# Kernel optimization log

Hardware: AMD Instinct MI355X
Metric: run time of the kernel (lower is better)

Reference implementation:

```python
import jax, jax.numpy as jnp
import numpy as np

COMMIT_W = 0.25
EMA_DECAY = 0.99
EPS = 1e-5


def setup_inputs() -> dict:
    key = jax.random.key(0)
    k1, k2 = jax.random.split(key)
    B, T, D, K = 16, 1024, 512, 8192
    features = jax.random.normal(k1, (B, T, D), dtype=jnp.float32)
    # __init__ does uniform_(-1/K, 1/K) then ema_weight.copy_(embeddings)
    embeddings = jax.random.uniform(k2, (K, D), dtype=jnp.float32, minval=-1.0 / K, maxval=1.0 / K)
    ema_weight = embeddings
    ema_cluster_size = jnp.ones((K,), dtype=jnp.float32)
    return {"features": features, "embeddings": embeddings,
            "ema_cluster_size": ema_cluster_size, "ema_weight": ema_weight}


def reference(features, embeddings, ema_cluster_size, ema_weight):
    B, T, D = features.shape
    K = embeddings.shape[0]
    flat = features.reshape(-1, D)                      # [N, D]
    # Squared-distance expansion; argmin is identical to argmin of cdist.
    d2 = (jnp.sum(flat * flat, axis=1, keepdims=True)
          - 2.0 * flat @ embeddings.T
          + jnp.sum(embeddings * embeddings, axis=1))   # [N, K]
    indices = jnp.argmin(d2, axis=1)                    # [N]
    quantized = embeddings[indices].reshape(B, T, D)
    # Straight-through estimator
    quantized_st = features + jax.lax.stop_gradient(quantized - features)
    commitment = jnp.mean((features - jax.lax.stop_gradient(quantized_st)) ** 2)
    extra_losses = COMMIT_W * commitment
    # EMA codebook update (training mode); scatter-add instead of one-hot matmul
    ones = jnp.ones(indices.shape, dtype=flat.dtype)
    cluster_size = jax.ops.segment_sum(ones, indices, num_segments=K)          # [K]
    embed_sum = jax.ops.segment_sum(jax.lax.stop_gradient(flat), indices,
                                    num_segments=K)                            # [K, D]
    new_cs = EMA_DECAY * ema_cluster_size + (1.0 - EMA_DECAY) * cluster_size
    new_w = EMA_DECAY * ema_weight + (1.0 - EMA_DECAY) * embed_sum
    cs_norm = (new_cs + EPS) / (jnp.sum(new_cs) + K * EPS)
    new_embeddings = new_w / cs_norm[:, None]
    targets = indices.reshape(B, T)
    return quantized_st, targets, extra_losses, new_embeddings, new_cs, new_w
```

## Files before the change

kernel.cpp:

```cpp
#include <hip/hip_runtime.h>

typedef unsigned short u16;
typedef unsigned int   u32;
typedef unsigned long long u64;

constexpr int NROW  = 16384;
constexpr int DIM   = 512;
constexpr int KCODE = 8192;

constexpr int BM   = 128;
constexpr int BN   = 128;
constexpr int BK   = 32;
constexpr int LSTR = 36;

constexpr size_t Q_OFF = 0;
constexpr size_t T_OFF = 8388608;
constexpr size_t L_OFF = 8404992;
constexpr size_t E_OFF = 8404993;
constexpr size_t C_OFF = 12599297;
constexpr size_t W_OFF = 12607489;

constexpr size_t WS_KEYS   = 0;
constexpr size_t WS_CSIZE  = 131072;
constexpr size_t WS_COMMIT = 163840;
constexpr size_t WS_CSSUM  = 163844;
constexpr size_t WS_XNORM  = 196608;
constexpr size_t WS_ENORM  = 262144;
constexpr size_t WS_ESUM   = 327680;
constexpr size_t WS_NEEDED = WS_ESUM + (size_t)KCODE * DIM * 4;

__global__ void rownorm_kernel(const float* __restrict__ src, float* __restrict__ dst) {
    #pragma clang fp contract(off)
    __shared__ float s[4][DIM];
    __shared__ float rr[4][32];
    const int wave = threadIdx.x >> 6, lane = threadIdx.x & 63;
    const int row = blockIdx.x * 4 + wave;
    const float4* p = (const float4*)(src + (size_t)row * DIM);
    float4 v0 = p[lane];
    float4 v1 = p[lane + 64];
    *(float4*)&s[wave][lane * 4] = v0;
    *(float4*)&s[wave][(lane + 64) * 4] = v1;
    __syncthreads();
    if (lane < 32) {
        const int b = lane >> 3, j = lane & 7;
        const float* q = &s[wave][b * 128 + j];
        float x = q[0];
        float r = x * x;
        for (int t = 1; t < 16; ++t) {
            float y = q[8 * t];
            float py = y * y;
            r = r + py;
        }
        rr[wave][lane] = r;
    }
    __syncthreads();
    if (lane == 0) {
        const float* R = rr[wave];
        float B0 = ((R[0] + R[1]) + (R[2] + R[3])) + ((R[4] + R[5]) + (R[6] + R[7]));
        float B1 = ((R[8] + R[9]) + (R[10] + R[11])) + ((R[12] + R[13]) + (R[14] + R[15]));
        float B2 = ((R[16] + R[17]) + (R[18] + R[19])) + ((R[20] + R[21]) + (R[22] + R[23]));
        float B3 = ((R[24] + R[25]) + (R[26] + R[27])) + ((R[28] + R[29]) + (R[30] + R[31]));
        dst[row] = (B0 + B1) + (B2 + B3);
    }
}

typedef short bf16x8 __attribute__((ext_vector_type(8)));
typedef float f32x16 __attribute__((ext_vector_type(16)));

__device__ __forceinline__ bf16x8 ld_frag(const u16* p) {
    uint2 a = *(const uint2*)p;
    uint2 b = *(const uint2*)(p + 4);
    int4 t = make_int4((int)a.x, (int)a.y, (int)b.x, (int)b.y);
    return __builtin_bit_cast(bf16x8, t);
}

__device__ __forceinline__ u32 bf16rne(float x) {
    u32 u = __float_as_uint(x);
    return (u + 0x7fffu + ((u >> 16) & 1u)) >> 16;
}

__device__ __forceinline__ void split4(float4 v, u32& hp0, u32& hp1, u32& lp0, u32& lp1) {
    u32 h0 = bf16rne(v.x), h1 = bf16rne(v.y), h2 = bf16rne(v.z), h3 = bf16rne(v.w);
    hp0 = h0 | (h1 << 16);
    hp1 = h2 | (h3 << 16);
    float r0 = v.x - __uint_as_float(h0 << 16);
    float r1 = v.y - __uint_as_float(h1 << 16);
    float r2 = v.z - __uint_as_float(h2 << 16);
    float r3 = v.w - __uint_as_float(h3 << 16);
    lp0 = bf16rne(r0) | (bf16rne(r1) << 16);
    lp1 = bf16rne(r2) | (bf16rne(r3) << 16);
}

__device__ __forceinline__ u64 packkey(float v, int code) {
    u32 vb = __float_as_uint(v);
    vb = (vb & 0x80000000u) ? ~vb : (vb | 0x80000000u);
    return ((u64)vb << 32) | (u32)code;
}

__launch_bounds__(256, 3)
__global__ void argmin_kernel(const float* __restrict__ feat,
                              const float* __restrict__ emb,
                              const float* __restrict__ xnorm,
                              const float* __restrict__ enorm,
                              u64* __restrict__ keys) {
    __shared__ u16 sAh[BM][LSTR], sAl[BM][LSTR], sBh[BN][LSTR], sBl[BN][LSTR];
    __shared__ float sXn[BM], sEn[BN];

    const int tid = threadIdx.x;
    const int swz = ((int)blockIdx.x & 7) * 1024 + ((int)blockIdx.x >> 3);
    const int cp = swz & 63;
    const int rp = swz >> 6;
    const int row0 = rp * BM;
    const int code0 = cp * BN;

    if (tid < BM) sXn[tid] = xnorm[row0 + tid];
    else          sEn[tid - BM] = enorm[code0 + (tid - BM)];

    const int srow = tid >> 3;
    const int scol = (tid & 7) * 4;
    const float* aBase = feat + (size_t)row0 * DIM;
    const float* bBase = emb + (size_t)code0 * DIM;

    float4 pa[4], pb[4];
    #pragma unroll
    for (int l = 0; l < 4; ++l) {
        pa[l] = *(const float4*)&aBase[(size_t)(srow + 32 * l) * DIM + scol];
        pb[l] = *(const float4*)&bBase[(size_t)(srow + 32 * l) * DIM + scol];
    }

    const int lane = tid & 63;
    const int wv = tid >> 6;
    const int wr = wv & 1, wc = wv >> 1;
    const int c5 = lane & 31, hgrp = lane >> 5;

    f32x16 acc[2][2] = {};

    #pragma unroll 1
    for (int kt = 0; kt < DIM / BK; ++kt) {
        __syncthreads();
        #pragma unroll
        for (int l = 0; l < 4; ++l) {
            u32 h0, h1, q0, q1;
            split4(pa[l], h0, h1, q0, q1);
            *(uint2*)&sAh[srow + 32 * l][scol] = make_uint2(h0, h1);
            *(uint2*)&sAl[srow + 32 * l][scol] = make_uint2(q0, q1);
            split4(pb[l], h0, h1, q0, q1);
            *(uint2*)&sBh[srow + 32 * l][scol] = make_uint2(h0, h1);
            *(uint2*)&sBl[srow + 32 * l][scol] = make_uint2(q0, q1);
        }
        __syncthreads();
        if (kt + 1 < DIM / BK) {
            const int k0 = (kt + 1) * BK;
            #pragma unroll
            for (int l = 0; l < 4; ++l) {
                pa[l] = *(const float4*)&aBase[(size_t)(srow + 32 * l) * DIM + k0 + scol];
                pb[l] = *(const float4*)&bBase[(size_t)(srow + 32 * l) * DIM + k0 + scol];
            }
        }
        #pragma unroll
        for (int s = 0; s < 2; ++s) {
            const int kk = s * 16 + hgrp * 8;
            bf16x8 ah[2], al[2], bh[2], bl[2];
            #pragma unroll
            for (int i = 0; i < 2; ++i) {
                ah[i] = ld_frag(&sAh[64 * wr + 32 * i + c5][kk]);
                al[i] = ld_frag(&sAl[64 * wr + 32 * i + c5][kk]);
                bh[i] = ld_frag(&sBh[64 * wc + 32 * i + c5][kk]);
                bl[i] = ld_frag(&sBl[64 * wc + 32 * i + c5][kk]);
            }
            #pragma unroll
            for (int i = 0; i < 2; ++i) {
                #pragma unroll
                for (int j = 0; j < 2; ++j) {
                    acc[i][j] = __builtin_amdgcn_mfma_f32_32x32x16_bf16(ah[i], bh[j], acc[i][j], 0, 0, 0);
                    acc[i][j] = __builtin_amdgcn_mfma_f32_32x32x16_bf16(ah[i], bl[j], acc[i][j], 0, 0, 0);
                    acc[i][j] = __builtin_amdgcn_mfma_f32_32x32x16_bf16(al[i], bh[j], acc[i][j], 0, 0, 0);
                }
            }
        }
    }

    #pragma unroll
    for (int i = 0; i < 2; ++i) {
        #pragma unroll
        for (int r = 0; r < 16; ++r) {
            const int rowt = 64 * wr + 32 * i + (r & 3) + 8 * (r >> 2) + 4 * hgrp;
            const float xv = sXn[rowt];
            const int ct0 = 64 * wc + c5;
            float v0 = fmaf(-2.0f, acc[i][0][r], xv) + sEn[ct0];
            float v1 = fmaf(-2.0f, acc[i][1][r], xv) + sEn[ct0 + 32];
            u64 ka = packkey(v0, code0 + ct0);
            u64 kb = packkey(v1, code0 + ct0 + 32);
            u64 key = (kb < ka) ? kb : ka;
            #pragma unroll
            for (int m = 1; m < 32; m <<= 1) {
                u64 o = __shfl_xor(key, m, 64);
                if (o < key) key = o;
            }
            if (c5 == 0) atomicMin(&keys[row0 + rowt], key);
        }
    }
}

__global__ void gather_kernel(const float* __restrict__ feat,
                              const float* __restrict__ emb,
                              const unsigned long long* __restrict__ keys,
                              float* __restrict__ qout,
                              float* __restrict__ targets,
                              float* __restrict__ esum,
                              float* __restrict__ csize,
                              float* __restrict__ commit) {
    const int row = blockIdx.x;
    const int code = (int)(keys[row] & 0x7fffffffu);
    const int d = threadIdx.x * 2;
    float2 f = *(const float2*)&feat[(size_t)row * DIM + d];
    float2 q = *(const float2*)&emb[(size_t)code * DIM + d];
    float2 qst;
    qst.x = f.x + (q.x - f.x);
    qst.y = f.y + (q.y - f.y);
    *(float2*)&qout[(size_t)row * DIM + d] = qst;
    float dx = f.x - qst.x, dy = f.y - qst.y;
    float local = dx * dx + dy * dy;
    #pragma unroll
    for (int off = 32; off; off >>= 1) local += __shfl_down(local, off, 64);
    __shared__ float wsum[4];
    int lane = threadIdx.x & 63, wv = threadIdx.x >> 6;
    if (lane == 0) wsum[wv] = local;
    __syncthreads();
    if (threadIdx.x == 0) {
        atomicAdd(commit, wsum[0] + wsum[1] + wsum[2] + wsum[3]);
        atomicAdd(&csize[code], 1.0f);
        targets[row] = (float)code;
    }
    atomicAdd(&esum[(size_t)code * DIM + d], f.x);
    atomicAdd(&esum[(size_t)code * DIM + d + 1], f.y);
}

__global__ void newcs_kernel(const float* __restrict__ ema_cs,
                             const float* __restrict__ csize,
                             float* __restrict__ out_cs,
                             float* __restrict__ cs_sum,
                             const float* __restrict__ commit,
                             float* __restrict__ out_loss) {
    int i = blockIdx.x * 256 + threadIdx.x;
    float v = 0.99f * ema_cs[i] + 0.01f * csize[i];
    out_cs[i] = v;
    float s = v;
    #pragma unroll
    for (int off = 32; off; off >>= 1) s += __shfl_down(s, off, 64);
    __shared__ float wsum[4];
    int lane = threadIdx.x & 63, wv = threadIdx.x >> 6;
    if (lane == 0) wsum[wv] = s;
    __syncthreads();
    if (threadIdx.x == 0)
        atomicAdd(cs_sum, wsum[0] + wsum[1] + wsum[2] + wsum[3]);
    if (blockIdx.x == 0 && threadIdx.x == 0)
        out_loss[0] = 0.25f * commit[0] / 8388608.0f;
}

__global__ void final_kernel(const float* __restrict__ ema_w,
                             const float* __restrict__ esum,
                             const float* __restrict__ new_cs,
                             const float* __restrict__ cs_sum,
                             float* __restrict__ out_w,
                             float* __restrict__ out_emb) {
    size_t i4 = ((size_t)blockIdx.x * 256 + threadIdx.x) * 4;
    int k = (int)(i4 >> 9);
    float S = cs_sum[0] + (float)KCODE * 1e-5f;
    float4 es = *(const float4*)&esum[i4];
    float4 ew = *(const float4*)&ema_w[i4];
    float w0 = 0.99f * ew.x + 0.01f * es.x;
    float w1 = 0.99f * ew.y + 0.01f * es.y;
    float w2 = 0.99f * ew.z + 0.01f * es.z;
    float w3 = 0.99f * ew.w + 0.01f * es.w;
    out_w[i4 + 0] = w0; out_w[i4 + 1] = w1; out_w[i4 + 2] = w2; out_w[i4 + 3] = w3;
    float scale = S / (new_cs[k] + 1e-5f);
    out_emb[i4 + 0] = w0 * scale; out_emb[i4 + 1] = w1 * scale;
    out_emb[i4 + 2] = w2 * scale; out_emb[i4 + 3] = w3 * scale;
}

extern "C" void kernel_launch(void* const* d_in, const int* in_sizes, int n_in,
                              void* d_out, int out_size, void* d_ws, size_t ws_size,
                              hipStream_t stream) {
    const float* feat   = (const float*)d_in[0];
    const float* emb    = (const float*)d_in[1];
    const float* ema_cs = (const float*)d_in[2];
    const float* ema_w  = (const float*)d_in[3];
    float* out = (float*)d_out;
    char* ws = (char*)d_ws;
    if (ws_size < WS_NEEDED) return;

    u64* keys     = (u64*)(ws + WS_KEYS);
    float* csize  = (float*)(ws + WS_CSIZE);
    float* commit = (float*)(ws + WS_COMMIT);
    float* cssum  = (float*)(ws + WS_CSSUM);
    float* xnorm  = (float*)(ws + WS_XNORM);
    float* enorm  = (float*)(ws + WS_ENORM);
    float* esum   = (float*)(ws + WS_ESUM);

    (void)hipMemsetAsync(ws + WS_KEYS, 0xFF, (size_t)NROW * 8, stream);
    (void)hipMemsetAsync(ws + WS_CSIZE, 0, WS_CSSUM + 4 - WS_CSIZE, stream);
    (void)hipMemsetAsync(ws + WS_ESUM, 0, (size_t)KCODE * DIM * 4, stream);

    rownorm_kernel<<<NROW / 4, 256, 0, stream>>>(feat, xnorm);
    rownorm_kernel<<<KCODE / 4, 256, 0, stream>>>(emb, enorm);
    argmin_kernel<<<(NROW / BM) * (KCODE / BN), 256, 0, stream>>>(feat, emb, xnorm, enorm, keys);
    gather_kernel<<<NROW, 256, 0, stream>>>(feat, emb, keys, out + Q_OFF, out + T_OFF,
                                            esum, csize, commit);
    newcs_kernel<<<KCODE / 256, 256, 0, stream>>>(ema_cs, csize, out + C_OFF, cssum, commit, out + L_OFF);
    final_kernel<<<KCODE * DIM / 1024, 256, 0, stream>>>(ema_w, esum, out + C_OFF, cssum,
                                                         out + W_OFF, out + E_OFF);
}
```

Baseline: 1.028 ms.

## Pre-split inputs into bf16 hi/lo buffers before the argmin GEMM

```diff
diff --git a/kernel.cpp b/kernel.cpp
--- a/kernel.cpp
+++ b/kernel.cpp
@@ -28,6 +28,11 @@
 constexpr size_t WS_ENORM  = 262144;
 constexpr size_t WS_ESUM   = 327680;
 constexpr size_t WS_NEEDED = WS_ESUM + (size_t)KCODE * DIM * 4;
+constexpr size_t WS_FH = WS_NEEDED;
+constexpr size_t WS_FL = WS_FH + (size_t)NROW * DIM * 2;
+constexpr size_t WS_EH = WS_FL + (size_t)NROW * DIM * 2;
+constexpr size_t WS_EL = WS_EH + (size_t)KCODE * DIM * 2;
+constexpr size_t WS_BIG = WS_EL + (size_t)KCODE * DIM * 2;
 
 __global__ void rownorm_kernel(const float* __restrict__ src, float* __restrict__ dst) {
     #pragma clang fp contract(off)
@@ -67,10 +72,7 @@
 typedef short bf16x8 __attribute__((ext_vector_type(8)));
 typedef float f32x16 __attribute__((ext_vector_type(16)));
 
-__device__ __forceinline__ bf16x8 ld_frag(const u16* p) {
-    uint2 a = *(const uint2*)p;
-    uint2 b = *(const uint2*)(p + 4);
-    int4 t = make_int4((int)a.x, (int)a.y, (int)b.x, (int)b.y);
+__device__ __forceinline__ bf16x8 frag_of(int4 t) {
     return __builtin_bit_cast(bf16x8, t);
 }
 
@@ -97,12 +99,135 @@
     return ((u64)vb << 32) | (u32)code;
 }
 
+__global__ void split_kernel(const float* __restrict__ src,
+                             u16* __restrict__ hi, u16* __restrict__ lo) {
+    const size_t i = (size_t)blockIdx.x * 256 + threadIdx.x;
+    const float4* p = (const float4*)src;
+    float4 a = p[i * 2], b = p[i * 2 + 1];
+    u32 ah0, ah1, al0, al1, bh0, bh1, bl0, bl1;
+    split4(a, ah0, ah1, al0, al1);
+    split4(b, bh0, bh1, bl0, bl1);
+    ((uint4*)hi)[i] = make_uint4(ah0, ah1, bh0, bh1);
+    ((uint4*)lo)[i] = make_uint4(al0, al1, bl0, bl1);
+}
+
 __launch_bounds__(256, 3)
-__global__ void argmin_kernel(const float* __restrict__ feat,
-                              const float* __restrict__ emb,
-                              const float* __restrict__ xnorm,
-                              const float* __restrict__ enorm,
-                              u64* __restrict__ keys) {
+__global__ void argmin_ps_kernel(const u16* __restrict__ fH, const u16* __restrict__ fL,
+                                 const u16* __restrict__ eH, const u16* __restrict__ eL,
+                                 const float* __restrict__ xnorm,
+                                 const float* __restrict__ enorm,
+                                 u64* __restrict__ keys) {
+    __shared__ int4 sAh[512], sAl[512], sBh[512], sBl[512];
+    __shared__ float sXn[BM], sEn[BN];
+
+    const int tid = threadIdx.x;
+    const int swz = ((int)blockIdx.x & 7) * 1024 + ((int)blockIdx.x >> 3);
+    const int cp = swz & 63;
+    const int rp = swz >> 6;
+    const int row0 = rp * BM;
+    const int code0 = cp * BN;
+
+    if (tid < BM) sXn[tid] = xnorm[row0 + tid];
+    else          sEn[tid - BM] = enorm[code0 + (tid - BM)];
+
+    const int k8l = tid & 3;
+    const int c5s = (tid >> 2) & 31;
+    const int rbs = tid >> 7;
+    const int4* fH4 = (const int4*)fH;
+    const int4* fL4 = (const int4*)fL;
+    const int4* eH4 = (const int4*)eH;
+    const int4* eL4 = (const int4*)eL;
+    const size_t rowA = (size_t)(row0 + rbs * 32 + c5s);
+    const size_t rowB = (size_t)(code0 + rbs * 32 + c5s);
+    const int ldsIdx0 = rbs * 128 + k8l * 32 + c5s;
+
+    int4 pAh[2], pAl[2], pBh[2], pBl[2];
+    #pragma unroll
+    for (int r = 0; r < 2; ++r) {
+        const size_t ia = (rowA + 64 * r) * 64 + k8l;
+        const size_t ib = (rowB + 64 * r) * 64 + k8l;
+        pAh[r] = fH4[ia]; pAl[r] = fL4[ia];
+        pBh[r] = eH4[ib]; pBl[r] = eL4[ib];
+    }
+
+    const int lane = tid & 63;
+    const int wv = tid >> 6;
+    const int wr = wv & 1, wc = wv >> 1;
+    const int c5 = lane & 31, hgrp = lane >> 5;
+
+    f32x16 acc[2][2] = {};
+
+    #pragma unroll 1
+    for (int kt = 0; kt < DIM / BK; ++kt) {
+        __syncthreads();
+        #pragma unroll
+        for (int r = 0; r < 2; ++r) {
+            sAh[ldsIdx0 + 256 * r] = pAh[r];
+            sAl[ldsIdx0 + 256 * r] = pAl[r];
+            sBh[ldsIdx0 + 256 * r] = pBh[r];
+            sBl[ldsIdx0 + 256 * r] = pBl[r];
+        }
+        __syncthreads();
+        if (kt + 1 < DIM / BK) {
+            #pragma unroll
+            for (int r = 0; r < 2; ++r) {
+                const size_t ia = (rowA + 64 * r) * 64 + (kt + 1) * 4 + k8l;
+                const size_t ib = (rowB + 64 * r) * 64 + (kt + 1) * 4 + k8l;
+                pAh[r] = fH4[ia]; pAl[r] = fL4[ia];
+                pBh[r] = eH4[ib]; pBl[r] = eL4[ib];
+            }
+        }
+        #pragma unroll
+        for (int s = 0; s < 2; ++s) {
+            const int k8 = s * 2 + hgrp;
+            bf16x8 ah[2], al[2], bh[2], bl[2];
+            #pragma unroll
+            for (int i = 0; i < 2; ++i) {
+                ah[i] = frag_of(sAh[((2 * wr + i) * 4 + k8) * 32 + c5]);
+                al[i] = frag_of(sAl[((2 * wr + i) * 4 + k8) * 32 + c5]);
+                bh[i] = frag_of(sBh[((2 * wc + i) * 4 + k8) * 32 + c5]);
+                bl[i] = frag_of(sBl[((2 * wc + i) * 4 + k8) * 32 + c5]);
+            }
+            #pragma unroll
+            for (int i = 0; i < 2; ++i) {
+                #pragma unroll
+                for (int j = 0; j < 2; ++j) {
+                    acc[i][j] = __builtin_amdgcn_mfma_f32_32x32x16_bf16(ah[i], bh[j], acc[i][j], 0, 0, 0);
+                    acc[i][j] = __builtin_amdgcn_mfma_f32_32x32x16_bf16(ah[i], bl[j], acc[i][j], 0, 0, 0);
+                    acc[i][j] = __builtin_amdgcn_mfma_f32_32x32x16_bf16(al[i], bh[j], acc[i][j], 0, 0, 0);
+                }
+            }
+        }
+    }
+
+    #pragma unroll
+    for (int i = 0; i < 2; ++i) {
+        #pragma unroll
+        for (int r = 0; r < 16; ++r) {
+            const int rowt = 64 * wr + 32 * i + (r & 3) + 8 * (r >> 2) + 4 * hgrp;
+            const float xv = sXn[rowt];
+            const int ct0 = 64 * wc + c5;
+            float v0 = fmaf(-2.0f, acc[i][0][r], xv) + sEn[ct0];
+            float v1 = fmaf(-2.0f, acc[i][1][r], xv) + sEn[ct0 + 32];
+            u64 ka = packkey(v0, code0 + ct0);
+            u64 kb = packkey(v1, code0 + ct0 + 32);
+            u64 key = (kb < ka) ? kb : ka;
+            #pragma unroll
+            for (int m = 1; m < 32; m <<= 1) {
+                u64 o = __shfl_xor(key, m, 64);
+                if (o < key) key = o;
+            }
+            if (c5 == 0) atomicMin(&keys[row0 + rowt], key);
+        }
+    }
+}
+
+__launch_bounds__(256, 3)
+__global__ void argmin_conv_kernel(const float* __restrict__ feat,
+                                   const float* __restrict__ emb,
+                                   const float* __restrict__ xnorm,
+                                   const float* __restrict__ enorm,
+                                   u64* __restrict__ keys) {
     __shared__ u16 sAh[BM][LSTR], sAl[BM][LSTR], sBh[BN][LSTR], sBl[BN][LSTR];
     __shared__ float sXn[BM], sEn[BN];
 
@@ -163,10 +288,18 @@
             bf16x8 ah[2], al[2], bh[2], bl[2];
             #pragma unroll
             for (int i = 0; i < 2; ++i) {
-                ah[i] = ld_frag(&sAh[64 * wr + 32 * i + c5][kk]);
-                al[i] = ld_frag(&sAl[64 * wr + 32 * i + c5][kk]);
-                bh[i] = ld_frag(&sBh[64 * wc + 32 * i + c5][kk]);
-                bl[i] = ld_frag(&sBl[64 * wc + 32 * i + c5][kk]);
+                uint2 a0 = *(const uint2*)&sAh[64 * wr + 32 * i + c5][kk];
+                uint2 a1 = *(const uint2*)&sAh[64 * wr + 32 * i + c5][kk + 4];
+                ah[i] = frag_of(make_int4(a0.x, a0.y, a1.x, a1.y));
+                uint2 c0 = *(const uint2*)&sAl[64 * wr + 32 * i + c5][kk];
+                uint2 c1 = *(const uint2*)&sAl[64 * wr + 32 * i + c5][kk + 4];
+                al[i] = frag_of(make_int4(c0.x, c0.y, c1.x, c1.y));
+                uint2 b0 = *(const uint2*)&sBh[64 * wc + 32 * i + c5][kk];
+                uint2 b1 = *(const uint2*)&sBh[64 * wc + 32 * i + c5][kk + 4];
+                bh[i] = frag_of(make_int4(b0.x, b0.y, b1.x, b1.y));
+                uint2 d0 = *(const uint2*)&sBl[64 * wc + 32 * i + c5][kk];
+                uint2 d1 = *(const uint2*)&sBl[64 * wc + 32 * i + c5][kk + 4];
+                bl[i] = frag_of(make_int4(d0.x, d0.y, d1.x, d1.y));
             }
             #pragma unroll
             for (int i = 0; i < 2; ++i) {
@@ -304,7 +437,21 @@
 
     rownorm_kernel<<<NROW / 4, 256, 0, stream>>>(feat, xnorm);
     rownorm_kernel<<<KCODE / 4, 256, 0, stream>>>(emb, enorm);
-    argmin_kernel<<<(NROW / BM) * (KCODE / BN), 256, 0, stream>>>(feat, emb, xnorm, enorm, keys);
+
+    if (ws_size >= WS_BIG) {
+        u16* fH = (u16*)(ws + WS_FH);
+        u16* fL = (u16*)(ws + WS_FL);
+        u16* eH = (u16*)(ws + WS_EH);
+        u16* eL = (u16*)(ws + WS_EL);
+        split_kernel<<<(NROW * DIM) / (256 * 8), 256, 0, stream>>>(feat, fH, fL);
+        split_kernel<<<(KCODE * DIM) / (256 * 8), 256, 0, stream>>>(emb, eH, eL);
+        argmin_ps_kernel<<<(NROW / BM) * (KCODE / BN), 256, 0, stream>>>(fH, fL, eH, eL,
+                                                                         xnorm, enorm, keys);
+    } else {
+        argmin_conv_kernel<<<(NROW / BM) * (KCODE / BN), 256, 0, stream>>>(feat, emb,
+                                                                           xnorm, enorm, keys);
+    }
+
     gather_kernel<<<NROW, 256, 0, stream>>>(feat, emb, keys, out + Q_OFF, out + T_OFF,
                                             esum, csize, commit);
     newcs_kernel<<<KCODE / 256, 256, 0, stream>>>(ema_cs, csize, out + C_OFF, cssum, commit, out + L_OFF);
```

Measured after the change: 2.244 ms. 2.18x slower.
